# Optimization experiments

Hardware: AMD Instinct MI355X
Metric: run time of the kernel (lower is better)

## Reference

```python
import jax, jax.numpy as jnp
import numpy as np

B, L, W = 4, 512, 256
VOCAB, E, H = 30000, 300, 768
N_LABELS = 6


def setup_inputs() -> dict:
    key = jax.random.key(0)
    ks = jax.random.split(key, 7)
    return {
        "word_seq": jax.random.randint(ks[0], (B, W), 0, VOCAB),
        "hidden_state": jax.random.normal(ks[1], (B, L, H), dtype=jnp.float32),
        "label_value_matrix": jax.random.randint(ks[2], (B, L, W), 0, N_LABELS),
        "emb_a": jax.random.normal(ks[3], (VOCAB, E), dtype=jnp.float32) * 0.02,
        "lin_w": jax.random.normal(ks[4], (E, H), dtype=jnp.float32) * 0.02,
        "lin_b": jax.random.normal(ks[5], (H,), dtype=jnp.float32) * 0.02,
        "emb_c": jax.random.normal(ks[6], (N_LABELS, H), dtype=jnp.float32) * 0.02,
    }


def reference(word_seq, hidden_state, label_value_matrix, emb_a, lin_w, lin_b, emb_c):
    temper = jnp.asarray(emb_c.shape[1], hidden_state.dtype) ** 0.5  # hidden_size ** 0.5
    # embedding_a lookup + linear projection: [B,W,E] -> [B,W,H]
    a = emb_a[word_seq] @ lin_w + lin_b
    # attention-style scores u = hidden_state @ a^T / temper : [B,L,W]
    u = jnp.einsum("blh,bwh->blw", hidden_state, a) / temper
    # masked exp-normalize WITHOUT max-subtraction (faithful to original)
    mask = jnp.clip(label_value_matrix, 0, 1).astype(u.dtype)
    delta_exp_u = jnp.exp(u) * mask
    p = delta_exp_u / (jnp.sum(delta_exp_u, axis=2, keepdims=True) + 1e-10)
    # embedding_c gather [B,L,W,H], weight by p and reduce over W -> [B,L,H]
    ec = emb_c[label_value_matrix]
    o = jnp.einsum("blw,blwh->blh", p, ec)
    return o
```

## Files before the change

kernel.cpp:

```cpp
#include <hip/hip_runtime.h>

#define BB 4
#define LL 512
#define WW 256
#define WP 264
#define EE 300
#define HH 768

typedef __attribute__((ext_vector_type(8))) short bf16x8;
typedef __attribute__((ext_vector_type(4))) float f32x4;

__device__ __forceinline__ short f2bf(float f) {
    union { float f; unsigned u; } v; v.f = f;
    unsigned r = (v.u + 0x7FFFu + ((v.u >> 16) & 1u)) >> 16;
    return (short)r;
}

__global__ __launch_bounds__(256, 1) void kA_a_gemm(
    const int*   __restrict__ word_seq,
    const float* __restrict__ emb_a,
    const float* __restrict__ lin_w,
    const float* __restrict__ lin_b,
    short*       __restrict__ aT)
{
    __shared__ short eaL[2][64 * 168];
    __shared__ short lwL[2][64 * 168];

    const int t  = threadIdx.x;
    const int m0 = (blockIdx.x & 15) * 64;
    const int n0 = (blockIdx.x >> 4) * 64;

    const int lane = t & 63, wv = t >> 6;
    const int l15 = lane & 15, l4 = lane >> 4;

    const int r_ea = t >> 2;
    const int q_ea = t & 3;
    const int h_lw = t & 63;
    const int q_lw = t >> 6;

    const int    wrow = word_seq[m0 + r_ea];
    const float* arow = emb_a + (long)wrow * EE;

    f32x4 acc[4] = {};
    float ea_reg[40], lw_reg[40];

#pragma unroll
    for (int half = 0; half < 2; ++half) {
        const int k0 = half * 160;
        {
            const int cbase = k0 + q_ea * 40;
#pragma unroll
            for (int c4 = 0; c4 < 10; ++c4) {
                const int col = cbase + c4 * 4;
                if (col <= 296) {
                    const float4 p = *(const float4*)(arow + col);
                    ea_reg[c4 * 4 + 0] = p.x; ea_reg[c4 * 4 + 1] = p.y;
                    ea_reg[c4 * 4 + 2] = p.z; ea_reg[c4 * 4 + 3] = p.w;
                } else {
                    ea_reg[c4 * 4 + 0] = 0.f; ea_reg[c4 * 4 + 1] = 0.f;
                    ea_reg[c4 * 4 + 2] = 0.f; ea_reg[c4 * 4 + 3] = 0.f;
                }
            }
            const int cb2 = k0 + q_lw * 40;
#pragma unroll
            for (int j = 0; j < 40; ++j) {
                const int col = cb2 + j;
                lw_reg[j] = (col < EE) ? lin_w[(long)col * HH + n0 + h_lw] : 0.f;
            }
        }
        {
            const int eoff = r_ea * 168 + q_ea * 40;
#pragma unroll
            for (int c8 = 0; c8 < 5; ++c8) {
                bf16x8 sv;
#pragma unroll
                for (int j = 0; j < 8; ++j) sv[j] = f2bf(ea_reg[c8 * 8 + j]);
                *(bf16x8*)(&eaL[half][eoff + c8 * 8]) = sv;
            }
            const int loff = h_lw * 168 + q_lw * 40;
#pragma unroll
            for (int c8 = 0; c8 < 5; ++c8) {
                bf16x8 sv;
#pragma unroll
                for (int j = 0; j < 8; ++j) sv[j] = f2bf(lw_reg[c8 * 8 + j]);
                *(bf16x8*)(&lwL[half][loff + c8 * 8]) = sv;
            }
        }
        __syncthreads();
#pragma unroll
        for (int ks = 0; ks < 5; ++ks) {
            const bf16x8 af =
                *(const bf16x8*)(&eaL[half][(wv * 16 + l15) * 168 + ks * 32 + l4 * 8]);
#pragma unroll
            for (int nf = 0; nf < 4; ++nf) {
                const bf16x8 bfv =
                    *(const bf16x8*)(&lwL[half][(nf * 16 + l15) * 168 + ks * 32 + l4 * 8]);
                acc[nf] = __builtin_amdgcn_mfma_f32_16x16x32_bf16(af, bfv, acc[nf], 0, 0, 0);
            }
        }
    }

    const int b1 = m0 >> 8;
#pragma unroll
    for (int nf = 0; nf < 4; ++nf) {
        const int h    = n0 + nf * 16 + l15;
        const float bv = lin_b[h];
        const long hbase = ((long)(b1 * 96 + (h >> 3)) * WP) * 8 + (h & 7);
#pragma unroll
        for (int i = 0; i < 4; ++i) {
            const int w = (m0 & 255) + wv * 16 + l4 * 4 + i;
            aT[hbase + (long)w * 8] = f2bf(acc[nf][i] + bv);
        }
    }
}

__global__ __launch_bounds__(512, 1) void kB_attn(
    const float* __restrict__ hidden,
    const int*   __restrict__ label,
    const short* __restrict__ aT,
    float*       __restrict__ s_part)
{
    __shared__ short hid[32 * 776];
    __shared__ float s_lds[4][2][16][5];

    const int t = threadIdx.x, lane = t & 63, wv = t >> 6;
    const int l15 = lane & 15, l4 = lane >> 4;
    const int mh = wv >> 2, wq = wv & 3;

    const int bid = blockIdx.x;
    const int xcd = bid & 7, j = bid >> 3;
    const int b   = xcd >> 1;
    const int lt  = j >> 1;
    const int ws  = ((xcd & 1) << 1) | (j & 1);
    const int row0 = b * 512 + lt * 32;
    const int wg   = ws * 64 + wq * 16 + l15;

    {
        const float* hrow = hidden + (long)row0 * HH;
#pragma unroll
        for (int jj = 0; jj < 6; ++jj) {
            const int ci  = t + jj * 512;
            const int row = ci / 96;
            const int col = (ci - row * 96) * 8;
            const float4 p0 = *(const float4*)(hrow + (long)row * HH + col);
            const float4 p1 = *(const float4*)(hrow + (long)row * HH + col + 4);
            bf16x8 v;
            v[0] = f2bf(p0.x); v[1] = f2bf(p0.y); v[2] = f2bf(p0.z); v[3] = f2bf(p0.w);
            v[4] = f2bf(p1.x); v[5] = f2bf(p1.y); v[6] = f2bf(p1.z); v[7] = f2bf(p1.w);
            *(bf16x8*)(&hid[row * 776 + col]) = v;
        }
    }

    int lv[4];
#pragma unroll
    for (int i = 0; i < 4; ++i)
        lv[i] = label[((long)row0 + mh * 16 + l4 * 4 + i) * WW + wg];
    __syncthreads();

    const short* abase = aT + (long)b * 96 * WP * 8;
    f32x4 acc = {};
#pragma unroll
    for (int ks = 0; ks < 24; ++ks) {
        const bf16x8 af =
            *(const bf16x8*)(&hid[(mh * 16 + l15) * 776 + ks * 32 + l4 * 8]);
        const bf16x8 bfv =
            *(const bf16x8*)(abase + ((long)(ks * 4 + l4) * WP + wg) * 8);
        acc = __builtin_amdgcn_mfma_f32_16x16x32_bf16(af, bfv, acc, 0, 0, 0);
    }

    const float inv_temper = 0.03608439182435161f;
    float s_loc[4][5];
#pragma unroll
    for (int i = 0; i < 4; ++i) {
        const float e = __expf(acc[i] * inv_temper);
#pragma unroll
        for (int c = 1; c <= 5; ++c)
            s_loc[i][c - 1] = (lv[i] == c) ? e : 0.f;
    }
#pragma unroll
    for (int i = 0; i < 4; ++i) {
#pragma unroll
        for (int c = 0; c < 5; ++c) {
            float v = s_loc[i][c];
            v += __shfl_xor(v, 1);
            v += __shfl_xor(v, 2);
            v += __shfl_xor(v, 4);
            v += __shfl_xor(v, 8);
            s_loc[i][c] = v;
        }
    }
    if (l15 == 0) {
#pragma unroll
        for (int i = 0; i < 4; ++i)
#pragma unroll
            for (int c = 0; c < 5; ++c)
                s_lds[wq][mh][l4 * 4 + i][c] = s_loc[i][c];
    }
    __syncthreads();
    if (t < 32) {
#pragma unroll
        for (int c = 0; c < 5; ++c) {
            const float s = s_lds[0][t >> 4][t & 15][c] + s_lds[1][t >> 4][t & 15][c] +
                            s_lds[2][t >> 4][t & 15][c] + s_lds[3][t >> 4][t & 15][c];
            s_part[((long)row0 + t) * 20 + ws * 5 + c] = s;
        }
    }
}

__global__ __launch_bounds__(256) void k3_out(
    const float* __restrict__ s_part,
    const float* __restrict__ emb_c,
    float*       __restrict__ out)
{
    const int t  = threadIdx.x;
    const int r0 = blockIdx.x * 4;

    float ecv[3][5];
#pragma unroll
    for (int q = 0; q < 3; ++q)
#pragma unroll
        for (int c = 0; c < 5; ++c)
            ecv[q][c] = emb_c[(c + 1) * HH + t + q * 256];

#pragma unroll
    for (int r = 0; r < 4; ++r) {
        const int row = r0 + r;
        const long sb = (long)row * 20;
        float s[5], den = 1e-10f;
#pragma unroll
        for (int c = 0; c < 5; ++c) {
            s[c] = s_part[sb + c] + s_part[sb + 5 + c] +
                   s_part[sb + 10 + c] + s_part[sb + 15 + c];
            den += s[c];
        }
        const float id = 1.0f / den;
        float* orow = out + (long)row * HH;
#pragma unroll
        for (int q = 0; q < 3; ++q) {
            const float v = s[0] * ecv[q][0] + s[1] * ecv[q][1] + s[2] * ecv[q][2] +
                            s[3] * ecv[q][3] + s[4] * ecv[q][4];
            orow[t + q * 256] = v * id;
        }
    }
}

extern "C" void kernel_launch(void* const* d_in, const int* in_sizes, int n_in,
                              void* d_out, int out_size, void* d_ws, size_t ws_size,
                              hipStream_t stream) {
    const int*   word_seq = (const int*)  d_in[0];
    const float* hidden   = (const float*)d_in[1];
    const int*   label    = (const int*)  d_in[2];
    const float* emb_a    = (const float*)d_in[3];
    const float* lin_w    = (const float*)d_in[4];
    const float* lin_b    = (const float*)d_in[5];
    const float* emb_c    = (const float*)d_in[6];
    float* out = (float*)d_out;

    short* aT     = (short*)d_ws;
    float* s_part = (float*)((char*)d_ws + 0x200000);

    kA_a_gemm<<<dim3(192), 256, 0, stream>>>(word_seq, emb_a, lin_w, lin_b, aT);
    kB_attn<<<dim3(256), 512, 0, stream>>>(hidden, label, aT, s_part);
    k3_out<<<dim3(512), 256, 0, stream>>>(s_part, emb_c, out);
}
```

Measured before the change: 22.88 us.

## Move hidden-state bf16 conversion into GEMM prep kernel and simplify attn layout

New measurement: 26.28 us. +14.8%, slower.

```diff
diff --git a/kernel.cpp b/kernel.cpp
--- a/kernel.cpp
+++ b/kernel.cpp
@@ -3,7 +3,6 @@
 #define BB 4
 #define LL 512
 #define WW 256
-#define WP 264
 #define EE 300
 #define HH 768
 
@@ -16,17 +15,34 @@
     return (short)r;
 }
 
-__global__ __launch_bounds__(256, 1) void kA_a_gemm(
+__global__ __launch_bounds__(256, 1) void kA_prep(
     const int*   __restrict__ word_seq,
     const float* __restrict__ emb_a,
     const float* __restrict__ lin_w,
     const float* __restrict__ lin_b,
-    short*       __restrict__ aT)
+    const float* __restrict__ hidden,
+    short*       __restrict__ aT,
+    short*       __restrict__ hidb)
 {
+    const int t = threadIdx.x;
+
+    {
+        const long cbase = (long)blockIdx.x * 1024 + t;
+#pragma unroll
+        for (int q = 0; q < 4; ++q) {
+            const long idx = (cbase + q * 256) * 8;
+            const float4 p0 = *(const float4*)(hidden + idx);
+            const float4 p1 = *(const float4*)(hidden + idx + 4);
+            bf16x8 v;
+            v[0] = f2bf(p0.x); v[1] = f2bf(p0.y); v[2] = f2bf(p0.z); v[3] = f2bf(p0.w);
+            v[4] = f2bf(p1.x); v[5] = f2bf(p1.y); v[6] = f2bf(p1.z); v[7] = f2bf(p1.w);
+            *(bf16x8*)(hidb + idx) = v;
+        }
+    }
+
     __shared__ short eaL[2][64 * 168];
     __shared__ short lwL[2][64 * 168];
 
-    const int t  = threadIdx.x;
     const int m0 = (blockIdx.x & 15) * 64;
     const int n0 = (blockIdx.x >> 4) * 64;
 
@@ -105,7 +121,7 @@
     for (int nf = 0; nf < 4; ++nf) {
         const int h    = n0 + nf * 16 + l15;
         const float bv = lin_b[h];
-        const long hbase = ((long)(b1 * 96 + (h >> 3)) * WP) * 8 + (h & 7);
+        const long hbase = ((long)(b1 * 96 + (h >> 3)) * WW) * 8 + (h & 7);
 #pragma unroll
         for (int i = 0; i < 4; ++i) {
             const int w = (m0 & 255) + wv * 16 + l4 * 4 + i;
@@ -115,7 +131,7 @@
 }
 
 __global__ __launch_bounds__(512, 1) void kB_attn(
-    const float* __restrict__ hidden,
+    const short* __restrict__ hidb,
     const int*   __restrict__ label,
     const short* __restrict__ aT,
     float*       __restrict__ s_part)
@@ -128,26 +144,21 @@
     const int mh = wv >> 2, wq = wv & 3;
 
     const int bid = blockIdx.x;
-    const int xcd = bid & 7, j = bid >> 3;
-    const int b   = xcd >> 1;
-    const int lt  = j >> 1;
-    const int ws  = ((xcd & 1) << 1) | (j & 1);
+    const int b  = bid >> 6;
+    const int lt = (bid >> 2) & 15;
+    const int ws = bid & 3;
     const int row0 = b * 512 + lt * 32;
     const int wg   = ws * 64 + wq * 16 + l15;
 
     {
-        const float* hrow = hidden + (long)row0 * HH;
+        const short* hrow = hidb + (long)row0 * HH;
 #pragma unroll
         for (int jj = 0; jj < 6; ++jj) {
             const int ci  = t + jj * 512;
             const int row = ci / 96;
             const int col = (ci - row * 96) * 8;
-            const float4 p0 = *(const float4*)(hrow + (long)row * HH + col);
-            const float4 p1 = *(const float4*)(hrow + (long)row * HH + col + 4);
-            bf16x8 v;
-            v[0] = f2bf(p0.x); v[1] = f2bf(p0.y); v[2] = f2bf(p0.z); v[3] = f2bf(p0.w);
-            v[4] = f2bf(p1.x); v[5] = f2bf(p1.y); v[6] = f2bf(p1.z); v[7] = f2bf(p1.w);
-            *(bf16x8*)(&hid[row * 776 + col]) = v;
+            *(bf16x8*)(&hid[row * 776 + col]) =
+                *(const bf16x8*)(hrow + (long)row * HH + col);
         }
     }
 
@@ -157,14 +168,14 @@
         lv[i] = label[((long)row0 + mh * 16 + l4 * 4 + i) * WW + wg];
     __syncthreads();
 
-    const short* abase = aT + (long)b * 96 * WP * 8;
+    const short* abase = aT + (long)b * 96 * WW * 8;
     f32x4 acc = {};
 #pragma unroll
     for (int ks = 0; ks < 24; ++ks) {
         const bf16x8 af =
             *(const bf16x8*)(&hid[(mh * 16 + l15) * 776 + ks * 32 + l4 * 8]);
         const bf16x8 bfv =
-            *(const bf16x8*)(abase + ((long)(ks * 4 + l4) * WP + wg) * 8);
+            *(const bf16x8*)(abase + ((long)(ks * 4 + l4) * WW + wg) * 8);
         acc = __builtin_amdgcn_mfma_f32_16x16x32_bf16(af, bfv, acc, 0, 0, 0);
     }
 
@@ -257,9 +268,11 @@
     float* out = (float*)d_out;
 
     short* aT     = (short*)d_ws;
-    float* s_part = (float*)((char*)d_ws + 0x200000);
-
-    kA_a_gemm<<<dim3(192), 256, 0, stream>>>(word_seq, emb_a, lin_w, lin_b, aT);
-    kB_attn<<<dim3(256), 512, 0, stream>>>(hidden, label, aT, s_part);
+    short* hidb   = (short*)((char*)d_ws + 0x180000);
+    float* s_part = (float*)((char*)d_ws + 0x480000);
+
+    kA_prep<<<dim3(192), 256, 0, stream>>>(word_seq, emb_a, lin_w, lin_b,
+                                           hidden, aT, hidb);
+    kB_attn<<<dim3(256), 512, 0, stream>>>(hidb, label, aT, s_part);
     k3_out<<<dim3(512), 256, 0, stream>>>(s_part, emb_c, out);
 }
```
